# Optimization experiments

Hardware: AMD Instinct MI355X
Metric: run time of the kernel (lower is better)

## Reference

```python
import jax, jax.numpy as jnp
import numpy as np

HIDDEN = 128
N_USER = 100000
N_REST = 50000
N_EDGE = 1000000


def setup_inputs() -> dict:
    key = jax.random.key(0)
    ks = jax.random.split(key, 10)
    h = HIDDEN
    def lin(kw, kb, fan_in, fan_out):
        s = 1.0 / np.sqrt(fan_in)
        W = jax.random.uniform(kw, (fan_out, fan_in), jnp.float32, -s, s)
        b = jax.random.uniform(kb, (fan_out,), jnp.float32, -s, s)
        return W, b
    W1, b1 = lin(ks[0], ks[1], 2 * h, h)
    W2, b2 = lin(ks[2], ks[3], h, h)
    W3, b3 = lin(ks[4], ks[5], h, 1)
    return {
        "z_user": jax.random.normal(ks[6], (N_USER, h), jnp.float32),
        "z_rest": jax.random.normal(ks[7], (N_REST, h), jnp.float32),
        "row": jax.random.randint(ks[8], (N_EDGE,), 0, N_USER, jnp.int64),
        "col": jax.random.randint(ks[9], (N_EDGE,), 0, N_REST, jnp.int64),
        "W1": W1, "b1": b1, "W2": W2, "b2": b2, "W3": W3, "b3": b3,
    }


def reference(z_user, z_rest, row, col, W1, b1, W2, b2, W3, b3):
    # Gather endpoint embeddings per edge and concat: [E, 2h]
    z = jnp.concatenate([z_user[row], z_rest[col]], axis=-1)
    z = jax.nn.relu(z @ W1.T + b1)          # [E, h]
    z = jax.nn.relu(z @ W2.T + b2)          # [E, h]
    z = z @ W3.T + b3                       # [E, 1]
    return z.reshape(-1)
```

## Files before the change

kernel.cpp:

```cpp
#include <hip/hip_runtime.h>

typedef _Float16 f16;
typedef _Float16 f16x8 __attribute__((ext_vector_type(8)));
typedef float    f32x4 __attribute__((ext_vector_type(4)));

#define H 128

__global__ __launch_bounds__(256) void convert_weights(
    const float* __restrict__ W1, const float* __restrict__ W2,
    f16* __restrict__ W1h, f16* __restrict__ W2h)
{
    const int gid    = blockIdx.x * 256 + threadIdx.x;
    const int fi_all = gid >> 6;
    const int lane   = gid & 63;
    const int lg = lane >> 4, lr = lane & 15;
    const float* src;
    f16* dst;
    if (fi_all < 64) {
        const int h = fi_all >> 5, kt = (fi_all >> 3) & 3, nt = fi_all & 7;
        src = W1 + (size_t)(lr + 16 * nt) * (2 * H) + h * H + kt * 32 + lg * 8;
        dst = W1h + fi_all * 512 + lane * 8;
    } else {
        const int fi = fi_all - 64;
        const int kt = fi >> 3, nt = fi & 7;
        src = W2 + (size_t)(lr + 16 * nt) * H + kt * 32 + lg * 8;
        dst = W2h + fi * 512 + lane * 8;
    }
    const float4 x0 = *(const float4*)src;
    const float4 x1 = *(const float4*)(src + 4);
    *(f16x8*)dst = (f16x8){(f16)x0.x, (f16)x0.y, (f16)x0.z, (f16)x0.w,
                           (f16)x1.x, (f16)x1.y, (f16)x1.z, (f16)x1.w};
}

__global__ __launch_bounds__(256) void precompute_kernel(
    const float* __restrict__ zu, const float* __restrict__ zr,
    const f16* __restrict__ W1h, const float* __restrict__ b1,
    f16* __restrict__ U, f16* __restrict__ R,
    int nU, int nR, int nUblk)
{
    const int bid  = blockIdx.x;
    const bool isU = bid < nUblk;
    const float* src  = isU ? zu : zr;
    f16*        dst   = isU ? U : R;
    const int   nrows = isU ? nU : nR;
    const int   base  = (isU ? bid : bid - nUblk) * 64;
    const int   hsel  = isU ? 0 : 32;

    const int tid  = threadIdx.x;
    const int wid  = tid >> 6;
    const int lane = tid & 63;
    const int lg   = lane >> 4;
    const int lr   = lane & 15;

    const int arow   = base + wid * 16 + lr;
    const int arow_c = arow < nrows ? arow : (nrows - 1);
    f16x8 afr[4];
    #pragma unroll
    for (int kt = 0; kt < 4; ++kt) {
        const float* p = src + (size_t)arow_c * H + kt * 32 + lg * 8;
        const float4 x0 = *(const float4*)p;
        const float4 x1 = *(const float4*)(p + 4);
        afr[kt] = (f16x8){(f16)x0.x, (f16)x0.y, (f16)x0.z, (f16)x0.w,
                          (f16)x1.x, (f16)x1.y, (f16)x1.z, (f16)x1.w};
    }

    f32x4 acc[8];
    #pragma unroll
    for (int nt = 0; nt < 8; ++nt) {
        const float b = isU ? b1[lr + 16 * nt] : 0.0f;
        acc[nt] = (f32x4){b, b, b, b};
    }

    #pragma unroll
    for (int kt = 0; kt < 4; ++kt) {
        f16x8 bf[8];
        #pragma unroll
        for (int nt = 0; nt < 8; ++nt)
            bf[nt] = *(const f16x8*)(W1h + (size_t)(hsel + kt * 8 + nt) * 512 + lane * 8);
        #pragma unroll
        for (int nt = 0; nt < 8; ++nt)
            acc[nt] = __builtin_amdgcn_mfma_f32_16x16x32_f16(afr[kt], bf[nt], acc[nt], 0, 0, 0);
    }

    __shared__ f16 lds[64][136];
    #pragma unroll
    for (int nt = 0; nt < 8; ++nt)
        #pragma unroll
        for (int r = 0; r < 4; ++r)
            lds[wid * 16 + lg * 4 + r][lr + 16 * nt] = (f16)acc[nt][r];
    __syncthreads();

    const int srow = tid >> 2, q = tid & 3;
    const int grow = base + srow;
    if (grow < nrows) {
        const uint4* s = (const uint4*)&lds[srow][q * 32];
        uint4* d = (uint4*)(dst + (size_t)grow * H + q * 32);
        d[0] = s[0];
        d[1] = s[1];
        d[2] = s[2];
        d[3] = s[3];
    }
}

__global__ __launch_bounds__(256, 2) void edge_kernel(
    const int* __restrict__ row, const int* __restrict__ col,
    const f16* __restrict__ U, const f16* __restrict__ R,
    const f16* __restrict__ W2h, const float* __restrict__ b2,
    const float* __restrict__ W3, const float* __restrict__ b3,
    float* __restrict__ out, int nEdge, int nTiles)
{
    const int tid  = threadIdx.x;
    const int wid  = tid >> 6;
    const int lane = tid & 63;
    const int lg   = lane >> 4;
    const int lr   = lane & 15;

    f16x8 w2f[4][8];
    #pragma unroll
    for (int kt = 0; kt < 4; ++kt)
        #pragma unroll
        for (int nt = 0; nt < 8; ++nt)
            w2f[kt][nt] = *(const f16x8*)(W2h + (size_t)(kt * 8 + nt) * 512 + lane * 8);

    float b2v[8], w3v[8];
    #pragma unroll
    for (int nt = 0; nt < 8; ++nt) {
        b2v[nt] = b2[lr + 16 * nt];
        w3v[nt] = W3[lr + 16 * nt];
    }
    const float b3s = b3[0];

    const int stride = gridDim.x;
    int t = blockIdx.x;
    if (t >= nTiles) return;

    int e  = t * 64 + wid * 16 + lr;
    int ec = e < nEdge ? e : (nEdge - 1);
    int ri = row[ec], ci = col[ec];
    f16x8 fr[4];
    #pragma unroll
    for (int kt = 0; kt < 4; ++kt) {
        const f16x8 u = *(const f16x8*)(U + (size_t)ri * H + kt * 32 + lg * 8);
        const f16x8 r = *(const f16x8*)(R + (size_t)ci * H + kt * 32 + lg * 8);
        f16x8 s = u + r;
        #pragma unroll
        for (int i = 0; i < 8; ++i) s[i] = s[i] > (f16)0 ? s[i] : (f16)0;
        fr[kt] = s;
    }
    int riN = 0, ciN = 0;
    {
        const int tn = t + stride;
        if (tn < nTiles) {
            int en = tn * 64 + wid * 16 + lr;
            en = en < nEdge ? en : (nEdge - 1);
            riN = row[en];
            ciN = col[en];
        }
    }

    while (true) {
        const int  tnext = t + stride;
        const bool more  = tnext < nTiles;

        f16x8 gu[4], gr[4];
        if (more) {
            #pragma unroll
            for (int kt = 0; kt < 4; ++kt) {
                gu[kt] = *(const f16x8*)(U + (size_t)riN * H + kt * 32 + lg * 8);
                gr[kt] = *(const f16x8*)(R + (size_t)ciN * H + kt * 32 + lg * 8);
            }
        }
        int riN2 = 0, ciN2 = 0;
        const int tnn = tnext + stride;
        if (more && tnn < nTiles) {
            int en2 = tnn * 64 + wid * 16 + lr;
            en2 = en2 < nEdge ? en2 : (nEdge - 1);
            riN2 = row[en2];
            ciN2 = col[en2];
        }

        f32x4 acc[8];
        #pragma unroll
        for (int nt = 0; nt < 8; ++nt) acc[nt] = (f32x4){b2v[nt], b2v[nt], b2v[nt], b2v[nt]};
        #pragma unroll
        for (int kt = 0; kt < 4; ++kt)
            #pragma unroll
            for (int nt = 0; nt < 8; ++nt)
                acc[nt] = __builtin_amdgcn_mfma_f32_16x16x32_f16(fr[kt], w2f[kt][nt], acc[nt], 0, 0, 0);

        float s0 = 0.f, s1 = 0.f, s2 = 0.f, s3 = 0.f;
        #pragma unroll
        for (int nt = 0; nt < 8; ++nt) {
            const f32x4 a = acc[nt];
            s0 += fmaxf(a[0], 0.f) * w3v[nt];
            s1 += fmaxf(a[1], 0.f) * w3v[nt];
            s2 += fmaxf(a[2], 0.f) * w3v[nt];
            s3 += fmaxf(a[3], 0.f) * w3v[nt];
        }
        #pragma unroll
        for (int m = 1; m < 16; m <<= 1) {
            s0 += __shfl_xor(s0, m);
            s1 += __shfl_xor(s1, m);
            s2 += __shfl_xor(s2, m);
            s3 += __shfl_xor(s3, m);
        }
        if (lr == 0) {
            const int ebase = t * 64 + wid * 16 + lg * 4;
            if (ebase + 0 < nEdge) out[ebase + 0] = s0 + b3s;
            if (ebase + 1 < nEdge) out[ebase + 1] = s1 + b3s;
            if (ebase + 2 < nEdge) out[ebase + 2] = s2 + b3s;
            if (ebase + 3 < nEdge) out[ebase + 3] = s3 + b3s;
        }

        if (!more) break;
        #pragma unroll
        for (int kt = 0; kt < 4; ++kt) {
            f16x8 s = gu[kt] + gr[kt];
            #pragma unroll
            for (int i = 0; i < 8; ++i) s[i] = s[i] > (f16)0 ? s[i] : (f16)0;
            fr[kt] = s;
        }
        riN = riN2;
        ciN = ciN2;
        t = tnext;
    }
}

#define TILE 16
__global__ __launch_bounds__(256) void edgedec_f32(
    const float* __restrict__ z_user, const float* __restrict__ z_rest,
    const int* __restrict__ row, const int* __restrict__ col,
    const float* __restrict__ W1, const float* __restrict__ b1,
    const float* __restrict__ W2, const float* __restrict__ b2,
    const float* __restrict__ W3, const float* __restrict__ b3,
    float* __restrict__ out, int nEdge)
{
    __shared__ float zt[TILE][2 * H];
    __shared__ float h1t[TILE][H];
    __shared__ float part[TILE][16];
    const int tid  = threadIdx.x;
    const int base = blockIdx.x * TILE;
    {
        const int e0 = tid >> 6, half = (tid >> 5) & 1, q = tid & 31;
        #pragma unroll
        for (int it = 0; it < TILE / 4; ++it) {
            const int e = e0 + it * 4, ge = base + e;
            if (ge < nEdge) {
                const float* src = half ? (z_rest + (size_t)col[ge] * H)
                                        : (z_user + (size_t)row[ge] * H);
                *(float4*)&zt[e][half * H + q * 4] = *(const float4*)(src + q * 4);
            }
        }
    }
    __syncthreads();
    const int j = tid & (H - 1), g = tid >> 7;
    float acc[8];
    {
        const float bj = b1[j];
        #pragma unroll
        for (int e = 0; e < 8; ++e) acc[e] = bj;
        const float4* wp = (const float4*)(W1 + (size_t)j * (2 * H));
        for (int k4 = 0; k4 < (2 * H) / 4; ++k4) {
            const float4 w = wp[k4];
            #pragma unroll
            for (int e = 0; e < 8; ++e) {
                const float4 z = *(const float4*)&zt[g * 8 + e][k4 * 4];
                acc[e] = fmaf(w.x, z.x, acc[e]); acc[e] = fmaf(w.y, z.y, acc[e]);
                acc[e] = fmaf(w.z, z.z, acc[e]); acc[e] = fmaf(w.w, z.w, acc[e]);
            }
        }
        #pragma unroll
        for (int e = 0; e < 8; ++e) h1t[g * 8 + e][j] = fmaxf(acc[e], 0.0f);
    }
    __syncthreads();
    {
        const float bj = b2[j];
        #pragma unroll
        for (int e = 0; e < 8; ++e) acc[e] = bj;
        const float4* wp = (const float4*)(W2 + (size_t)j * H);
        for (int k4 = 0; k4 < H / 4; ++k4) {
            const float4 w = wp[k4];
            #pragma unroll
            for (int e = 0; e < 8; ++e) {
                const float4 h = *(const float4*)&h1t[g * 8 + e][k4 * 4];
                acc[e] = fmaf(w.x, h.x, acc[e]); acc[e] = fmaf(w.y, h.y, acc[e]);
                acc[e] = fmaf(w.z, h.z, acc[e]); acc[e] = fmaf(w.w, h.w, acc[e]);
            }
        }
        const float w3j = W3[j];
        __syncthreads();
        #pragma unroll
        for (int e = 0; e < 8; ++e) h1t[g * 8 + e][j] = w3j * fmaxf(acc[e], 0.0f);
    }
    __syncthreads();
    {
        const int e = tid >> 4, p = tid & 15;
        float s = 0.0f;
        #pragma unroll
        for (int i = 0; i < 8; ++i) s += h1t[e][p * 8 + i];
        part[e][p] = s;
    }
    __syncthreads();
    if (tid < TILE) {
        const int ge = base + tid;
        if (ge < nEdge) {
            float s = b3[0];
            #pragma unroll
            for (int i = 0; i < 16; ++i) s += part[tid][i];
            out[ge] = s;
        }
    }
}

extern "C" void kernel_launch(void* const* d_in, const int* in_sizes, int n_in,
                              void* d_out, int out_size, void* d_ws, size_t ws_size,
                              hipStream_t stream) {
    const float* z_user = (const float*)d_in[0];
    const float* z_rest = (const float*)d_in[1];
    const int*   row    = (const int*)d_in[2];
    const int*   col    = (const int*)d_in[3];
    const float* W1     = (const float*)d_in[4];
    const float* b1     = (const float*)d_in[5];
    const float* W2     = (const float*)d_in[6];
    const float* b2     = (const float*)d_in[7];
    const float* W3     = (const float*)d_in[8];
    const float* b3     = (const float*)d_in[9];
    float* out = (float*)d_out;

    const int nU    = in_sizes[0] / H;
    const int nR    = in_sizes[1] / H;
    const int nEdge = in_sizes[2];

    const size_t uBytes  = (size_t)nU * H * sizeof(f16);
    const size_t rBytes  = (size_t)nR * H * sizeof(f16);
    const size_t w2Bytes = (size_t)H * H * sizeof(f16);
    const size_t w1Bytes = (size_t)H * 2 * H * sizeof(f16);
    const size_t need    = uBytes + rBytes + w2Bytes + w1Bytes;

    if (ws_size < need) {
        const int nBlocks = (nEdge + TILE - 1) / TILE;
        hipLaunchKernelGGL(edgedec_f32, dim3(nBlocks), dim3(256), 0, stream,
                           z_user, z_rest, row, col, W1, b1, W2, b2, W3, b3, out, nEdge);
        return;
    }

    f16* U   = (f16*)d_ws;
    f16* R   = (f16*)((char*)d_ws + uBytes);
    f16* W2h = (f16*)((char*)d_ws + uBytes + rBytes);
    f16* W1h = (f16*)((char*)d_ws + uBytes + rBytes + w2Bytes);

    hipLaunchKernelGGL(convert_weights, dim3(24), dim3(256), 0, stream,
                       W1, W2, W1h, W2h);

    const int nUblk = (nU + 63) / 64;
    const int nRblk = (nR + 63) / 64;
    hipLaunchKernelGGL(precompute_kernel, dim3(nUblk + nRblk), dim3(256), 0, stream,
                       z_user, z_rest, W1h, b1, U, R, nU, nR, nUblk);

    const int nTiles = (nEdge + 63) / 64;
    const int grid   = nTiles < 1024 ? nTiles : 1024;
    hipLaunchKernelGGL(edge_kernel, dim3(grid), dim3(256), 0, stream,
                       row, col, U, R, W2h, b2, W3, b3, out, nEdge, nTiles);
}
```

Measured before the change: 118.5 us.

## Bucket-sort edges by user row to improve gather locality in edge MLP

Adds a histogram, scan and scatter pass that buckets the edges by row index into 1024 coarse buckets. The sorted edge kernel then gathers the U embeddings with better cache locality and writes each output through the original edge index. This aims to cut the cost of scattered global reads for the user-side gather. In exchange it adds four small kernel launches, atomic-heavy scatter traffic and indirect output writes. The random column gathers stay unsorted.

Result: slower. 378.3 us (+219.2%).

```diff
diff --git a/kernel.cpp b/kernel.cpp
--- a/kernel.cpp
+++ b/kernel.cpp
@@ -5,6 +5,7 @@
 typedef float    f32x4 __attribute__((ext_vector_type(4)));
 
 #define H 128
+#define NB 1024
 
 __global__ __launch_bounds__(256) void convert_weights(
     const float* __restrict__ W1, const float* __restrict__ W2,
@@ -102,6 +103,205 @@
     }
 }
 
+__global__ __launch_bounds__(256) void zero_hist(unsigned* __restrict__ g)
+{
+    g[blockIdx.x * 256 + threadIdx.x] = 0u;
+}
+
+__global__ __launch_bounds__(256) void hist_kernel(
+    const int* __restrict__ row, unsigned* __restrict__ ghist, int nEdge, int shift)
+{
+    __shared__ unsigned h[NB];
+    for (int i = threadIdx.x; i < NB; i += 256) h[i] = 0u;
+    __syncthreads();
+    int i = blockIdx.x * 256 + threadIdx.x;
+    const int stride = gridDim.x * 256;
+    for (; i < nEdge; i += stride) atomicAdd(&h[row[i] >> shift], 1u);
+    __syncthreads();
+    for (int i = threadIdx.x; i < NB; i += 256)
+        if (h[i]) atomicAdd(&ghist[i], h[i]);
+}
+
+__global__ __launch_bounds__(1024) void scan_kernel(
+    const unsigned* __restrict__ ghist,
+    unsigned* __restrict__ bucketCur)
+{
+    __shared__ unsigned a[NB], b[NB];
+    const int tid = threadIdx.x;
+    a[tid] = ghist[tid];
+    __syncthreads();
+    unsigned* src = a;
+    unsigned* dst = b;
+    for (int off = 1; off < NB; off <<= 1) {
+        const unsigned v = src[tid] + (tid >= off ? src[tid - off] : 0u);
+        dst[tid] = v;
+        __syncthreads();
+        unsigned* t = src; src = dst; dst = t;
+    }
+    bucketCur[tid] = tid ? src[tid - 1] : 0u;
+}
+
+__global__ __launch_bounds__(256) void scatter_kernel(
+    const int* __restrict__ row, const int* __restrict__ col,
+    unsigned* __restrict__ cur,
+    int* __restrict__ sRow, int* __restrict__ sCol, int* __restrict__ sIdx,
+    int nEdge, int shift)
+{
+    int i = blockIdx.x * 256 + threadIdx.x;
+    const int stride = gridDim.x * 256;
+    for (; i < nEdge; i += stride) {
+        const int r = row[i], c = col[i];
+        const unsigned slot = atomicAdd(&cur[r >> shift], 1u);
+        sRow[slot] = r;
+        sCol[slot] = c;
+        sIdx[slot] = i;
+    }
+}
+
+__global__ __launch_bounds__(256, 2) void edge_kernel_sorted(
+    const int* __restrict__ sRow, const int* __restrict__ sCol,
+    const int* __restrict__ sIdx,
+    const f16* __restrict__ U, const f16* __restrict__ R,
+    const f16* __restrict__ W2h, const float* __restrict__ b2,
+    const float* __restrict__ W3, const float* __restrict__ b3,
+    float* __restrict__ out, int nEdge, int nTiles)
+{
+    const int tid  = threadIdx.x;
+    const int wid  = tid >> 6;
+    const int lane = tid & 63;
+    const int lg   = lane >> 4;
+    const int lr   = lane & 15;
+
+    f16x8 w2f[4][8];
+    #pragma unroll
+    for (int kt = 0; kt < 4; ++kt)
+        #pragma unroll
+        for (int nt = 0; nt < 8; ++nt)
+            w2f[kt][nt] = *(const f16x8*)(W2h + (size_t)(kt * 8 + nt) * 512 + lane * 8);
+
+    float b2v[8], w3v[8];
+    #pragma unroll
+    for (int nt = 0; nt < 8; ++nt) {
+        b2v[nt] = b2[lr + 16 * nt];
+        w3v[nt] = W3[lr + 16 * nt];
+    }
+    const float b3s = b3[0];
+
+    const int stride = gridDim.x;
+    int t = blockIdx.x;
+    if (t >= nTiles) return;
+
+    auto load_oi = [&](int tt) -> int4 {
+        int4 v = {0, 0, 0, 0};
+        if (lr == 0) {
+            const int eb = tt * 64 + wid * 16 + lg * 4;
+            if (eb + 3 < nEdge) v = *(const int4*)&sIdx[eb];
+            else {
+                v.x = sIdx[eb + 0 < nEdge ? eb + 0 : nEdge - 1];
+                v.y = sIdx[eb + 1 < nEdge ? eb + 1 : nEdge - 1];
+                v.z = sIdx[eb + 2 < nEdge ? eb + 2 : nEdge - 1];
+                v.w = sIdx[eb + 3 < nEdge ? eb + 3 : nEdge - 1];
+            }
+        }
+        return v;
+    };
+
+    int e  = t * 64 + wid * 16 + lr;
+    int ec = e < nEdge ? e : (nEdge - 1);
+    int ri = sRow[ec], ci = sCol[ec];
+    int4 oi = load_oi(t);
+    f16x8 fr[4];
+    #pragma unroll
+    for (int kt = 0; kt < 4; ++kt) {
+        const f16x8 u = *(const f16x8*)(U + (size_t)ri * H + kt * 32 + lg * 8);
+        const f16x8 r = *(const f16x8*)(R + (size_t)ci * H + kt * 32 + lg * 8);
+        f16x8 s = u + r;
+        #pragma unroll
+        for (int i = 0; i < 8; ++i) s[i] = s[i] > (f16)0 ? s[i] : (f16)0;
+        fr[kt] = s;
+    }
+    int riN = 0, ciN = 0;
+    {
+        const int tn = t + stride;
+        if (tn < nTiles) {
+            int en = tn * 64 + wid * 16 + lr;
+            en = en < nEdge ? en : (nEdge - 1);
+            riN = sRow[en];
+            ciN = sCol[en];
+        }
+    }
+
+    while (true) {
+        const int  tnext = t + stride;
+        const bool more  = tnext < nTiles;
+
+        f16x8 gu[4], gr[4];
+        int4 oiN = {0, 0, 0, 0};
+        if (more) {
+            #pragma unroll
+            for (int kt = 0; kt < 4; ++kt) {
+                gu[kt] = *(const f16x8*)(U + (size_t)riN * H + kt * 32 + lg * 8);
+                gr[kt] = *(const f16x8*)(R + (size_t)ciN * H + kt * 32 + lg * 8);
+            }
+            oiN = load_oi(tnext);
+        }
+        int riN2 = 0, ciN2 = 0;
+        const int tnn = tnext + stride;
+        if (more && tnn < nTiles) {
+            int en2 = tnn * 64 + wid * 16 + lr;
+            en2 = en2 < nEdge ? en2 : (nEdge - 1);
+            riN2 = sRow[en2];
+            ciN2 = sCol[en2];
+        }
+
+        f32x4 acc[8];
+        #pragma unroll
+        for (int nt = 0; nt < 8; ++nt) acc[nt] = (f32x4){b2v[nt], b2v[nt], b2v[nt], b2v[nt]};
+        #pragma unroll
+        for (int kt = 0; kt < 4; ++kt)
+            #pragma unroll
+            for (int nt = 0; nt < 8; ++nt)
+                acc[nt] = __builtin_amdgcn_mfma_f32_16x16x32_f16(fr[kt], w2f[kt][nt], acc[nt], 0, 0, 0);
+
+        float s0 = 0.f, s1 = 0.f, s2 = 0.f, s3 = 0.f;
+        #pragma unroll
+        for (int nt = 0; nt < 8; ++nt) {
+            const f32x4 a = acc[nt];
+            s0 += fmaxf(a[0], 0.f) * w3v[nt];
+            s1 += fmaxf(a[1], 0.f) * w3v[nt];
+            s2 += fmaxf(a[2], 0.f) * w3v[nt];
+            s3 += fmaxf(a[3], 0.f) * w3v[nt];
+        }
+        #pragma unroll
+        for (int m = 1; m < 16; m <<= 1) {
+            s0 += __shfl_xor(s0, m);
+            s1 += __shfl_xor(s1, m);
+            s2 += __shfl_xor(s2, m);
+            s3 += __shfl_xor(s3, m);
+        }
+        if (lr == 0) {
+            const int ebase = t * 64 + wid * 16 + lg * 4;
+            if (ebase + 0 < nEdge) out[oi.x] = s0 + b3s;
+            if (ebase + 1 < nEdge) out[oi.y] = s1 + b3s;
+            if (ebase + 2 < nEdge) out[oi.z] = s2 + b3s;
+            if (ebase + 3 < nEdge) out[oi.w] = s3 + b3s;
+        }
+
+        if (!more) break;
+        #pragma unroll
+        for (int kt = 0; kt < 4; ++kt) {
+            f16x8 s = gu[kt] + gr[kt];
+            #pragma unroll
+            for (int i = 0; i < 8; ++i) s[i] = s[i] > (f16)0 ? s[i] : (f16)0;
+            fr[kt] = s;
+        }
+        riN = riN2;
+        ciN = ciN2;
+        oi  = oiN;
+        t   = tnext;
+    }
+}
+
 __global__ __launch_bounds__(256, 2) void edge_kernel(
     const int* __restrict__ row, const int* __restrict__ col,
     const f16* __restrict__ U, const f16* __restrict__ R,
@@ -161,7 +361,6 @@
     while (true) {
         const int  tnext = t + stride;
         const bool more  = tnext < nTiles;
-
         f16x8 gu[4], gr[4];
         if (more) {
             #pragma unroll
@@ -335,30 +534,57 @@
     const size_t rBytes  = (size_t)nR * H * sizeof(f16);
     const size_t w2Bytes = (size_t)H * H * sizeof(f16);
     const size_t w1Bytes = (size_t)H * 2 * H * sizeof(f16);
-    const size_t need    = uBytes + rBytes + w2Bytes + w1Bytes;
-
-    if (ws_size < need) {
+    const size_t base    = uBytes + rBytes + w2Bytes + w1Bytes;
+    const size_t histB   = (size_t)NB * sizeof(unsigned);
+    const size_t idxB    = (size_t)nEdge * sizeof(int);
+    const size_t needSrt = base + 2 * histB + 3 * idxB;
+
+    if (ws_size < base) {
         const int nBlocks = (nEdge + TILE - 1) / TILE;
         hipLaunchKernelGGL(edgedec_f32, dim3(nBlocks), dim3(256), 0, stream,
                            z_user, z_rest, row, col, W1, b1, W2, b2, W3, b3, out, nEdge);
         return;
     }
 
-    f16* U   = (f16*)d_ws;
-    f16* R   = (f16*)((char*)d_ws + uBytes);
-    f16* W2h = (f16*)((char*)d_ws + uBytes + rBytes);
-    f16* W1h = (f16*)((char*)d_ws + uBytes + rBytes + w2Bytes);
+    char* p   = (char*)d_ws;
+    f16*  U   = (f16*)p;                       p += uBytes;
+    f16*  R   = (f16*)p;                       p += rBytes;
+    f16*  W2h = (f16*)p;                       p += w2Bytes;
+    f16*  W1h = (f16*)p;                       p += w1Bytes;
 
     hipLaunchKernelGGL(convert_weights, dim3(24), dim3(256), 0, stream,
                        W1, W2, W1h, W2h);
 
     const int nUblk = (nU + 63) / 64;
     const int nRblk = (nR + 63) / 64;
+    const int nTiles = (nEdge + 63) / 64;
+    const int grid   = nTiles < 1024 ? nTiles : 1024;
+
+    if (ws_size < needSrt) {
+        hipLaunchKernelGGL(precompute_kernel, dim3(nUblk + nRblk), dim3(256), 0, stream,
+                           z_user, z_rest, W1h, b1, U, R, nU, nR, nUblk);
+        hipLaunchKernelGGL(edge_kernel, dim3(grid), dim3(256), 0, stream,
+                           row, col, U, R, W2h, b2, W3, b3, out, nEdge, nTiles);
+        return;
+    }
+
+    unsigned* ghist = (unsigned*)p;            p += histB;
+    unsigned* bcur  = (unsigned*)p;            p += histB;
+    int* sRow = (int*)p;                       p += idxB;
+    int* sCol = (int*)p;                       p += idxB;
+    int* sIdx = (int*)p;                       p += idxB;
+
+    int shift = 0;
+    while (((unsigned)(nU - 1) >> shift) >= NB) ++shift;
+
+    hipLaunchKernelGGL(zero_hist, dim3(NB / 256), dim3(256), 0, stream, ghist);
+    hipLaunchKernelGGL(hist_kernel, dim3(512), dim3(256), 0, stream,
+                       row, ghist, nEdge, shift);
+    hipLaunchKernelGGL(scan_kernel, dim3(1), dim3(NB), 0, stream, ghist, bcur);
     hipLaunchKernelGGL(precompute_kernel, dim3(nUblk + nRblk), dim3(256), 0, stream,
                        z_user, z_rest, W1h, b1, U, R, nU, nR, nUblk);
-
-    const int nTiles = (nEdge + 63) / 64;
-    const int grid   = nTiles < 1024 ? nTiles : 1024;
-    hipLaunchKernelGGL(edge_kernel, dim3(grid), dim3(256), 0, stream,
-                       row, col, U, R, W2h, b2, W3, b3, out, nEdge, nTiles);
-}
+    hipLaunchKernelGGL(scatter_kernel, dim3(1024), dim3(256), 0, stream,
+                       row, col, bcur, sRow, sCol, sIdx, nEdge, shift);
+    hipLaunchKernelGGL(edge_kernel_sorted, dim3(grid), dim3(256), 0, stream,
+                       sRow, sCol, sIdx, U, R, W2h, b2, W3, b3, out, nEdge, nTiles);
+}
```
